# Kernel tuning notes

Measured on AMD Instinct MI355X. Metric: run time of the kernel, lower is better.

Reference implementation:

```python
import jax, jax.numpy as jnp
import numpy as np

V, E, HID, T = 50000, 256, 512, 12   # vocab, embed dim, lstm hidden (bi total), tagset size
START, STOP = 10, 11
L = 2048                              # sentence length
H = HID // 2                          # per-direction hidden
NEG = -10000.0


def setup_inputs():
    key = jax.random.key(0)
    ks = jax.random.split(key, 13)
    s = 0.05
    sentence = jax.random.randint(ks[0], (L,), 0, V)
    embed = jax.random.normal(ks[1], (V, E), jnp.float32) * s
    w_ih_f = jax.random.normal(ks[2], (4 * H, E), jnp.float32) * s
    w_hh_f = jax.random.normal(ks[3], (4 * H, H), jnp.float32) * s
    b_ih_f = jax.random.normal(ks[4], (4 * H,), jnp.float32) * s
    b_hh_f = jax.random.normal(ks[5], (4 * H,), jnp.float32) * s
    w_ih_b = jax.random.normal(ks[6], (4 * H, E), jnp.float32) * s
    w_hh_b = jax.random.normal(ks[7], (4 * H, H), jnp.float32) * s
    b_ih_b = jax.random.normal(ks[8], (4 * H,), jnp.float32) * s
    b_hh_b = jax.random.normal(ks[9], (4 * H,), jnp.float32) * s
    w_out = jax.random.normal(ks[10], (T, HID), jnp.float32) * s
    b_out = jax.random.normal(ks[11], (T,), jnp.float32) * s
    transitions = jax.random.normal(ks[12], (T, T), jnp.float32)
    transitions = transitions.at[START, :].set(NEG).at[:, STOP].set(NEG)
    return dict(sentence=sentence, embed=embed,
                w_ih_f=w_ih_f, w_hh_f=w_hh_f, b_ih_f=b_ih_f, b_hh_f=b_hh_f,
                w_ih_b=w_ih_b, w_hh_b=w_hh_b, b_ih_b=b_ih_b, b_hh_b=b_hh_b,
                w_out=w_out, b_out=b_out, transitions=transitions)


def _lstm_dir(x, w_ih, w_hh, b, reverse):
    # x: [L, E] -> hs: [L, H]; PyTorch gate order i, f, g, o
    xg = x @ w_ih.T + b  # [L, 4H] precomputed input contribution

    def step(carry, xg_t):
        h, c = carry
        g = xg_t + h @ w_hh.T
        i, f, gg, o = jnp.split(g, 4)
        i, f, o = jax.nn.sigmoid(i), jax.nn.sigmoid(f), jax.nn.sigmoid(o)
        c = f * c + i * jnp.tanh(gg)
        h = o * jnp.tanh(c)
        return (h, c), h

    hdim = w_hh.shape[1]
    init = (jnp.zeros((hdim,), x.dtype), jnp.zeros((hdim,), x.dtype))
    _, hs = jax.lax.scan(step, init, xg, reverse=reverse)
    return hs


def _lstm_feats(sentence, embed, w_ih_f, w_hh_f, b_ih_f, b_hh_f,
                w_ih_b, w_hh_b, b_ih_b, b_hh_b, w_out, b_out):
    x = embed[sentence]                                        # [L, E]
    hf = _lstm_dir(x, w_ih_f, w_hh_f, b_ih_f + b_hh_f, False)  # [L, H]
    hb = _lstm_dir(x, w_ih_b, w_hh_b, b_ih_b + b_hh_b, True)   # [L, H]
    h = jnp.concatenate([hf, hb], axis=-1)                     # [L, 2H]
    return h @ w_out.T + b_out                                 # [L, T]


def reference(sentence, embed, w_ih_f, w_hh_f, b_ih_f, b_hh_f,
              w_ih_b, w_hh_b, b_ih_b, b_hh_b, w_out, b_out, transitions):
    feats = _lstm_feats(sentence, embed, w_ih_f, w_hh_f, b_ih_f, b_hh_f,
                        w_ih_b, w_hh_b, b_ih_b, b_hh_b, w_out, b_out)

    # Viterbi DP vectorized over tags, scanned over time
    init_v = jnp.full((T,), NEG, feats.dtype).at[START].set(0.0)

    def vstep(v, feat):
        scores = transitions + v[None, :]        # [next_tag, prev_tag]
        bp = jnp.argmax(scores, axis=1)          # best previous tag per next tag
        v_new = jnp.max(scores, axis=1) + feat
        return v_new, bp

    v, bps = jax.lax.scan(vstep, init_v, feats)  # bps: [L, T]
    terminal = v + transitions[STOP]
    best = jnp.argmax(terminal)
    path_score = terminal[best]

    def btrack(tag, bp):
        return bp[tag], tag

    _, best_path = jax.lax.scan(btrack, best, bps, reverse=True)  # [L] tags
    return path_score, best_path
```

## Files before the change

kernel.cpp:

```cpp
#include <hip/hip_runtime.h>

#define LSEQ 2048
#define TAGS 12

typedef _Float16 half2v __attribute__((ext_vector_type(2)));
typedef unsigned long long u64;

__device__ __forceinline__ float sigm(float x){ return 1.0f/(1.0f+__expf(-x)); }
__device__ __forceinline__ float tanh_fast(float x){ return 1.0f - 2.0f/(1.0f+__expf(2.0f*x)); }
__device__ __forceinline__ half2v pack2(float a, float b){
  half2v r; r.x=(_Float16)a; r.y=(_Float16)b; return r;
}

__device__ __forceinline__ void wg_barrier(){
  asm volatile("s_waitcnt lgkmcnt(0)" ::: "memory");
  __builtin_amdgcn_s_barrier();
  __builtin_amdgcn_sched_barrier(0);
  asm volatile("" ::: "memory");
}

__global__ void init_kernel(u64* ex)
{
  int tid = blockIdx.x*256 + threadIdx.x;
  if (tid < 1024) ex[tid] = 0ull;
}

__global__ void xg_kernel(
    const int* sent, const float* embed,
    const float* w_ih_f, const float* b_ih_f, const float* b_hh_f,
    const float* w_ih_b, const float* b_ih_b, const float* b_hh_b,
    float* xg)
{
  __shared__ float x_sh[8][256];
  int tid = threadIdx.x;
  int t0 = blockIdx.x * 8;
  for (int i=0;i<8;++i){
    int idx = sent[t0+i];
    x_sh[i][tid] = embed[(size_t)idx*256 + tid];
  }
  __syncthreads();
  for (int ri=0; ri<8; ++ri){
    int r = ri*256 + tid;
    int d = r >> 10;
    int row = r & 1023;
    const float* wr = (d ? w_ih_b : w_ih_f) + (size_t)row*256;
    const float* bi = d ? b_ih_b : b_ih_f;
    const float* bh = d ? b_hh_b : b_hh_f;
    float acc[8];
    #pragma unroll
    for (int i=0;i<8;++i) acc[i]=0.f;
    for (int k0=0;k0<256;k0+=4){
      float4 p = *(const float4*)(wr + k0);
      #pragma unroll
      for (int i=0;i<8;++i){
        acc[i] += p.x*x_sh[i][k0] + p.y*x_sh[i][k0+1]
                + p.z*x_sh[i][k0+2] + p.w*x_sh[i][k0+3];
      }
    }
    float bias = bi[row] + bh[row];
    #pragma unroll
    for (int i=0;i<8;++i)
      xg[((size_t)d*LSEQ + (size_t)(t0+i))*1024 + row] = acc[i] + bias;
  }
}

__global__ __launch_bounds__(256,1) void lstm_rec(
    const float* __restrict__ w_hh_f, const float* __restrict__ w_hh_b,
    const float* __restrict__ xg, unsigned short* __restrict__ hstH,
    u64* __restrict__ ex)
{
  int blk = blockIdx.x;
  int d = blk & 7;
  if (d > 1) return;
  int q = blk >> 3;
  int qa = (q+1)&3, qb = (q+2)&3, qc = (q+3)&3;

  int tid = threadIdx.x;
  int g = tid >> 6, l = tid & 63;
  int row = g*256 + 64*q + l;
  const float* W = d ? w_hh_b : w_hh_f;
  const float* xgd = xg + (size_t)d*LSEQ*1024;
  unsigned short* hd = hstH + (size_t)d*LSEQ*256;
  u64* exd = ex + (size_t)d*256;

  __shared__ float gate_sh[2][256];
  __shared__ unsigned h2all[128];

  half2v w[128];
  {
    const float* p0 = W + (size_t)row*256 + 64*q;
    const float* p1 = W + (size_t)row*256 + 64*qa;
    const float* p2 = W + (size_t)row*256 + 64*qb;
    const float* p3 = W + (size_t)row*256 + 64*qc;
    #pragma unroll
    for (int k0=0;k0<16;++k0){
      float4 a = *(const float4*)(p0+4*k0);
      w[2*k0]      = pack2(a.x,a.y);  w[2*k0+1]    = pack2(a.z,a.w);
      float4 b = *(const float4*)(p1+4*k0);
      w[32+2*k0]   = pack2(b.x,b.y);  w[32+2*k0+1] = pack2(b.z,b.w);
      float4 cc= *(const float4*)(p2+4*k0);
      w[64+2*k0]   = pack2(cc.x,cc.y); w[64+2*k0+1] = pack2(cc.z,cc.w);
      float4 e = *(const float4*)(p3+4*k0);
      w[96+2*k0]   = pack2(e.x,e.y);  w[96+2*k0+1] = pack2(e.z,e.w);
    }
  }
  if (tid < 128) h2all[tid] = 0u;
  float c0 = 0.f, c1 = 0.f;
  unsigned hp = 0u;

  int pollj = tid - 64;
  int pollpeer = (q + 1 + (pollj>>5)) & 3;
  int pollslot = 32*pollpeer + (pollj & 31);
  int adrA = (l < 32) ? (32*qa + l) : (32*qb + (l-32));
  int adrB = 32*qc + (l & 31);
  bool is_pub  = (tid < 32);
  bool is_poll = (tid >= 64) && (tid < 160);
  __syncthreads();

  int tf = d ? (LSEQ-1) : 0;
  float xg0 = xgd[(size_t)tf*1024 + row];

  for (int s=0;s<LSEQ;++s){
    u64 v0 = 0ull;
    bool p = is_poll && (s > 0);
    if (p)
      v0 = __hip_atomic_load(&exd[((s&1)<<7) + pollslot],
                             __ATOMIC_RELAXED, __HIP_MEMORY_SCOPE_AGENT);
    float a0=xg0, a1=0.f, a2=0.f, a3=0.f;
    #pragma unroll
    for (int k=0;k<32;k+=4){
      unsigned p0v = __builtin_amdgcn_readlane(hp,k);
      unsigned p1v = __builtin_amdgcn_readlane(hp,k+1);
      unsigned p2v = __builtin_amdgcn_readlane(hp,k+2);
      unsigned p3v = __builtin_amdgcn_readlane(hp,k+3);
      a0 = __builtin_amdgcn_fdot2(__builtin_bit_cast(half2v,p0v), w[k],   a0, false);
      a1 = __builtin_amdgcn_fdot2(__builtin_bit_cast(half2v,p1v), w[k+1], a1, false);
      a2 = __builtin_amdgcn_fdot2(__builtin_bit_cast(half2v,p2v), w[k+2], a2, false);
      a3 = __builtin_amdgcn_fdot2(__builtin_bit_cast(half2v,p3v), w[k+3], a3, false);
    }
    float nxg = 0.f;
    if (s+1 < LSEQ){
      int tn = d ? (LSEQ-2-s) : (s+1);
      nxg = xgd[(size_t)tn*1024 + row];
    }
    if (p){
      u64 v = v0;
      while ((unsigned)(v>>32) != (unsigned)s)
        v = __hip_atomic_load(&exd[((s&1)<<7) + pollslot],
                              __ATOMIC_RELAXED, __HIP_MEMORY_SCOPE_AGENT);
      h2all[pollslot] = (unsigned)v;
    }
    wg_barrier();
    unsigned hrA = h2all[adrA];
    unsigned hrB = h2all[adrB];
    #pragma unroll
    for (int k=0;k<32;k+=2){
      unsigned pA0 = __builtin_amdgcn_readlane(hrA, k);
      unsigned pA1 = __builtin_amdgcn_readlane(hrA, k+1);
      unsigned pB0 = __builtin_amdgcn_readlane(hrA, 32+k);
      unsigned pB1 = __builtin_amdgcn_readlane(hrA, 32+k+1);
      unsigned pC0 = __builtin_amdgcn_readlane(hrB, k);
      unsigned pC1 = __builtin_amdgcn_readlane(hrB, k+1);
      a0 = __builtin_amdgcn_fdot2(__builtin_bit_cast(half2v,pA0), w[32+k],   a0, false);
      a1 = __builtin_amdgcn_fdot2(__builtin_bit_cast(half2v,pA1), w[32+k+1], a1, false);
      a2 = __builtin_amdgcn_fdot2(__builtin_bit_cast(half2v,pB0), w[64+k],   a2, false);
      a3 = __builtin_amdgcn_fdot2(__builtin_bit_cast(half2v,pB1), w[64+k+1], a3, false);
      a0 = __builtin_amdgcn_fdot2(__builtin_bit_cast(half2v,pC0), w[96+k],   a0, false);
      a1 = __builtin_amdgcn_fdot2(__builtin_bit_cast(half2v,pC1), w[96+k+1], a1, false);
    }
    float pre = (a0+a1) + (a2+a3);
    float act = (g==2) ? tanh_fast(pre) : sigm(pre);
    gate_sh[s&1][tid] = act;
    wg_barrier();
    {
      int m = l & 31;
      const float* gp = gate_sh[s&1];
      float2 gi = *(const float2*)&gp[      2*m];
      float2 gf = *(const float2*)&gp[ 64 + 2*m];
      float2 gg = *(const float2*)&gp[128 + 2*m];
      float2 go = *(const float2*)&gp[192 + 2*m];
      c0 = gf.x*c0 + gi.x*gg.x;
      c1 = gf.y*c1 + gi.y*gg.y;
      float h0 = go.x * tanh_fast(c0);
      float h1 = go.y * tanh_fast(c1);
      hp = __builtin_bit_cast(unsigned, pack2(h0,h1));
    }
    if (is_pub){
      if (s+1 < LSEQ)
        atomicExch(&exd[(((s+1)&1)<<7) + 32*q + tid],
                   ((u64)(unsigned)(s+1) << 32) | (u64)hp);
      int tp = d ? (LSEQ-1-s) : s;
      *(unsigned*)&hd[(size_t)tp*256 + 64*q + 2*tid] = hp;
    }
    xg0 = nxg;
  }
}

__global__ void feats_kernel(
    const unsigned short* hstH, const float* w_out, const float* b_out,
    float* feats)
{
  __shared__ float w_sh[12*520];
  __shared__ float h_sh[16*520];
  const _Float16* hf = (const _Float16*)hstH;
  int tid=threadIdx.x;
  int t0=blockIdx.x*16;
  for (int i=tid;i<12*512;i+=256){ int tag=i>>9,k=i&511; w_sh[tag*520+k]=w_out[i]; }
  for (int i=tid;i<16*512;i+=256){
    int tt=i>>9,k=i&511;
    float v = (k<256)? (float)hf[(size_t)(t0+tt)*256+k]
                     : (float)hf[(size_t)(LSEQ+t0+tt)*256 + (k-256)];
    h_sh[tt*520+k]=v;
  }
  __syncthreads();
  if (tid<192){
    int tt=tid/12, tag=tid%12;
    const float* wr=&w_sh[tag*520];
    const float* hr=&h_sh[tt*520];
    float acc=b_out[tag];
    for (int k=0;k<512;k+=4){
      float4 a=*(const float4*)(wr+k);
      float4 b=*(const float4*)(hr+k);
      acc += a.x*b.x+a.y*b.y+a.z*b.z+a.w*b.w;
    }
    feats[(size_t)(t0+tt)*12+tag]=acc;
  }
}

__global__ void BiLSTM_CRF_14405320311361_kernel(
    const float* feats, const float* trans, float* outp)
{
  __shared__ float fsh[LSEQ*12];
  __shared__ unsigned char bps[LSEQ*12];
  __shared__ float term_sh[16];
  __shared__ int ibuf[66];
  __shared__ unsigned char fmap[64*12];
  int tid = threadIdx.x;
  for (int i=tid; i<LSEQ*12/4; i+=256)
    *(float4*)&fsh[4*i] = *(const float4*)&feats[4*i];
  __syncthreads();

  int lane = tid & 63;
  int fl = (lane<12) ? lane : 0;
  float vn = 0.f;
  if (tid < 64){
    float tr[12];
    #pragma unroll
    for (int p=0;p<12;++p) tr[p] = trans[fl*12+p];
    vn = (lane==10) ? 0.f : -10000.f;
    float fa = fsh[fl];
    float fb = fsh[12+fl];
    for (int t=0;t<LSEQ;++t){
      unsigned vu = __float_as_uint(vn);
      float best; int bp; float sc;
      best = tr[0] + __uint_as_float(__builtin_amdgcn_readlane(vu,0)); bp = 0;
      sc = tr[1]  + __uint_as_float(__builtin_amdgcn_readlane(vu,1));  if(sc>best){best=sc;bp=1;}
      sc = tr[2]  + __uint_as_float(__builtin_amdgcn_readlane(vu,2));  if(sc>best){best=sc;bp=2;}
      sc = tr[3]  + __uint_as_float(__builtin_amdgcn_readlane(vu,3));  if(sc>best){best=sc;bp=3;}
      sc = tr[4]  + __uint_as_float(__builtin_amdgcn_readlane(vu,4));  if(sc>best){best=sc;bp=4;}
      sc = tr[5]  + __uint_as_float(__builtin_amdgcn_readlane(vu,5));  if(sc>best){best=sc;bp=5;}
      sc = tr[6]  + __uint_as_float(__builtin_amdgcn_readlane(vu,6));  if(sc>best){best=sc;bp=6;}
      sc = tr[7]  + __uint_as_float(__builtin_amdgcn_readlane(vu,7));  if(sc>best){best=sc;bp=7;}
      sc = tr[8]  + __uint_as_float(__builtin_amdgcn_readlane(vu,8));  if(sc>best){best=sc;bp=8;}
      sc = tr[9]  + __uint_as_float(__builtin_amdgcn_readlane(vu,9));  if(sc>best){best=sc;bp=9;}
      sc = tr[10] + __uint_as_float(__builtin_amdgcn_readlane(vu,10)); if(sc>best){best=sc;bp=10;}
      sc = tr[11] + __uint_as_float(__builtin_amdgcn_readlane(vu,11)); if(sc>best){best=sc;bp=11;}
      vn = best + fa;
      fa = fb;
      if (t+2 < LSEQ) fb = fsh[(t+2)*12+fl];
      if (lane<12) bps[t*12+lane] = (unsigned char)bp;
    }
  }
  if (tid < 12) term_sh[tid] = vn + trans[11*12+tid];
  __syncthreads();
  if (tid == 0){
    float bs=term_sh[0]; int bt=0;
    for (int p=1;p<12;++p){ if (term_sh[p]>bs){bs=term_sh[p];bt=p;} }
    outp[0] = bs;
    ibuf[64] = bt;
  }
  __syncthreads();
  if (tid < 64){
    int b = tid;
    int f[12];
    int thi = b*32+31;
    #pragma unroll
    for (int x=0;x<12;++x) f[x] = bps[thi*12+x];
    for (int t=thi-1; t>=b*32; --t){
      int base = t*12;
      #pragma unroll
      for (int x=0;x<12;++x) f[x] = bps[base + f[x]];
    }
    #pragma unroll
    for (int x=0;x<12;++x) fmap[b*12+x] = (unsigned char)f[x];
  }
  __syncthreads();
  if (tid == 0){
    int tag = ibuf[64];
    for (int b=63;b>=0;--b){ ibuf[b]=tag; tag = fmap[b*12+tag]; }
  }
  __syncthreads();
  if (tid < 64){
    int b = tid;
    int tag = ibuf[b];
    for (int t=b*32+31; t>=b*32; --t){
      outp[1+t] = (float)tag;
      tag = bps[t*12+tag];
    }
  }
}

extern "C" void kernel_launch(void* const* d_in, const int* in_sizes, int n_in,
                              void* d_out, int out_size, void* d_ws, size_t ws_size,
                              hipStream_t stream) {
  const int*   sent   = (const int*)d_in[0];
  const float* embed  = (const float*)d_in[1];
  const float* w_ih_f = (const float*)d_in[2];
  const float* w_hh_f = (const float*)d_in[3];
  const float* b_ih_f = (const float*)d_in[4];
  const float* b_hh_f = (const float*)d_in[5];
  const float* w_ih_b = (const float*)d_in[6];
  const float* w_hh_b = (const float*)d_in[7];
  const float* b_ih_b = (const float*)d_in[8];
  const float* b_hh_b = (const float*)d_in[9];
  const float* w_out  = (const float*)d_in[10];
  const float* b_out  = (const float*)d_in[11];
  const float* trans  = (const float*)d_in[12];

  float* xg = (float*)d_ws;
  unsigned short* hstH = (unsigned short*)(xg + (size_t)2*LSEQ*1024);
  u64* ex = (u64*)(hstH + (size_t)2*LSEQ*256);
  float* feats = (float*)(ex + 1024);
  float* outp  = (float*)d_out;

  init_kernel<<<dim3(4), dim3(256), 0, stream>>>(ex);
  xg_kernel<<<dim3(LSEQ/8), dim3(256), 0, stream>>>(
      sent, embed, w_ih_f, b_ih_f, b_hh_f, w_ih_b, b_ih_b, b_hh_b, xg);
  lstm_rec<<<dim3(32), dim3(256), 0, stream>>>(w_hh_f, w_hh_b, xg, hstH, ex);
  feats_kernel<<<dim3(LSEQ/16), dim3(256), 0, stream>>>(hstH, w_out, b_out, feats);
  BiLSTM_CRF_14405320311361_kernel<<<dim3(1), dim3(256), 0, stream>>>(feats, trans, outp);
}
```

Measured before the change: 3.577 ms.

## Split LSTM recurrence across two workgroups per direction with LDS-resident weight spill

Reduces the recurrent LSTM from four cooperating workgroups per direction to two, each owning 128 hidden units and computing two gate rows per thread. The remote half of the hidden state is exchanged through one global flag/data slot per lane instead of three peers, so cross-workgroup sync traffic and fan-in shrink. Register-held weights only partly fit, so 96 of the remote-half weight columns per row are stored in LDS as packed fp16 and read each step. The cost is more dot-product work per thread and LDS reads on the critical path, traded for fewer inter-block handshakes.

```diff
diff --git a/kernel.cpp b/kernel.cpp
--- a/kernel.cpp
+++ b/kernel.cpp
@@ -4,6 +4,7 @@
 #define TAGS 12
 
 typedef _Float16 half2v __attribute__((ext_vector_type(2)));
+typedef unsigned u32x4 __attribute__((ext_vector_type(4)));
 typedef unsigned long long u64;
 
 __device__ __forceinline__ float sigm(float x){ return 1.0f/(1.0f+__expf(-x)); }
@@ -11,6 +12,7 @@
 __device__ __forceinline__ half2v pack2(float a, float b){
   half2v r; r.x=(_Float16)a; r.y=(_Float16)b; return r;
 }
+__device__ __forceinline__ half2v h2(unsigned u){ return __builtin_bit_cast(half2v, u); }
 
 __device__ __forceinline__ void wg_barrier(){
   asm volatile("s_waitcnt lgkmcnt(0)" ::: "memory");
@@ -72,113 +74,137 @@
   int blk = blockIdx.x;
   int d = blk & 7;
   if (d > 1) return;
-  int q = blk >> 3;
-  int qa = (q+1)&3, qb = (q+2)&3, qc = (q+3)&3;
-
+  int c = blk >> 3;
   int tid = threadIdx.x;
-  int g = tid >> 6, l = tid & 63;
-  int row = g*256 + 64*q + l;
+  int uu = tid & 127;
+  int gp = tid >> 7;
+  int l  = tid & 63;
+  int u  = 128*c + uu;
+  int row0 = gp*256 + u;
+  int row1 = (gp+2)*256 + u;
+  int lr0 = gp*128 + uu;
+  int lr1 = (gp+2)*128 + uu;
   const float* W = d ? w_hh_b : w_hh_f;
   const float* xgd = xg + (size_t)d*LSEQ*1024;
   unsigned short* hd = hstH + (size_t)d*LSEQ*256;
   u64* exd = ex + (size_t)d*256;
 
-  __shared__ float gate_sh[2][256];
-  __shared__ unsigned h2all[128];
-
-  half2v w[128];
+  __shared__ unsigned wlds[12][512][4];
+  __shared__ float gate_sh[2][512];
+  __shared__ unsigned h2rem[2][64];
+
+  half2v wA[80], wB[80];
   {
-    const float* p0 = W + (size_t)row*256 + 64*q;
-    const float* p1 = W + (size_t)row*256 + 64*qa;
-    const float* p2 = W + (size_t)row*256 + 64*qb;
-    const float* p3 = W + (size_t)row*256 + 64*qc;
-    #pragma unroll
-    for (int k0=0;k0<16;++k0){
-      float4 a = *(const float4*)(p0+4*k0);
-      w[2*k0]      = pack2(a.x,a.y);  w[2*k0+1]    = pack2(a.z,a.w);
-      float4 b = *(const float4*)(p1+4*k0);
-      w[32+2*k0]   = pack2(b.x,b.y);  w[32+2*k0+1] = pack2(b.z,b.w);
-      float4 cc= *(const float4*)(p2+4*k0);
-      w[64+2*k0]   = pack2(cc.x,cc.y); w[64+2*k0+1] = pack2(cc.z,cc.w);
-      float4 e = *(const float4*)(p3+4*k0);
-      w[96+2*k0]   = pack2(e.x,e.y);  w[96+2*k0+1] = pack2(e.z,e.w);
-    }
-  }
-  if (tid < 128) h2all[tid] = 0u;
+    const float* pr0 = W + (size_t)row0*256;
+    const float* pr1 = W + (size_t)row1*256;
+    int ob = 128*c, pb = 128*(1-c);
+    #pragma unroll
+    for (int k2=0;k2<32;++k2){
+      float4 a = *(const float4*)(pr0 + ob + 4*k2);
+      wA[2*k2] = pack2(a.x,a.y); wA[2*k2+1] = pack2(a.z,a.w);
+      float4 b = *(const float4*)(pr1 + ob + 4*k2);
+      wB[2*k2] = pack2(b.x,b.y); wB[2*k2+1] = pack2(b.z,b.w);
+    }
+    #pragma unroll
+    for (int k2=0;k2<8;++k2){
+      float4 a = *(const float4*)(pr0 + pb + 4*k2);
+      wA[64+2*k2] = pack2(a.x,a.y); wA[64+2*k2+1] = pack2(a.z,a.w);
+      float4 b = *(const float4*)(pr1 + pb + 4*k2);
+      wB[64+2*k2] = pack2(b.x,b.y); wB[64+2*k2+1] = pack2(b.z,b.w);
+    }
+    for (int jg=0;jg<12;++jg){
+      float4 a0 = *(const float4*)(pr0 + pb + 32 + 8*jg);
+      float4 a1 = *(const float4*)(pr0 + pb + 32 + 8*jg + 4);
+      wlds[jg][lr0][0] = __builtin_bit_cast(unsigned, pack2(a0.x,a0.y));
+      wlds[jg][lr0][1] = __builtin_bit_cast(unsigned, pack2(a0.z,a0.w));
+      wlds[jg][lr0][2] = __builtin_bit_cast(unsigned, pack2(a1.x,a1.y));
+      wlds[jg][lr0][3] = __builtin_bit_cast(unsigned, pack2(a1.z,a1.w));
+      float4 b0 = *(const float4*)(pr1 + pb + 32 + 8*jg);
+      float4 b1 = *(const float4*)(pr1 + pb + 32 + 8*jg + 4);
+      wlds[jg][lr1][0] = __builtin_bit_cast(unsigned, pack2(b0.x,b0.y));
+      wlds[jg][lr1][1] = __builtin_bit_cast(unsigned, pack2(b0.z,b0.w));
+      wlds[jg][lr1][2] = __builtin_bit_cast(unsigned, pack2(b1.x,b1.y));
+      wlds[jg][lr1][3] = __builtin_bit_cast(unsigned, pack2(b1.z,b1.w));
+    }
+  }
+  if (tid < 128) h2rem[tid>>6][tid&63] = 0u;
   float c0 = 0.f, c1 = 0.f;
   unsigned hp = 0u;
-
-  int pollj = tid - 64;
-  int pollpeer = (q + 1 + (pollj>>5)) & 3;
-  int pollslot = 32*pollpeer + (pollj & 31);
-  int adrA = (l < 32) ? (32*qa + l) : (32*qb + (l-32));
-  int adrB = 32*qc + (l & 31);
-  bool is_pub  = (tid < 32);
-  bool is_poll = (tid >= 64) && (tid < 160);
+  bool is_pub  = (tid < 64);
+  bool is_poll = (tid >= 64) && (tid < 128);
   __syncthreads();
 
   int tf = d ? (LSEQ-1) : 0;
-  float xg0 = xgd[(size_t)tf*1024 + row];
+  float xga = xgd[(size_t)tf*1024 + row0];
+  float xgb = xgd[(size_t)tf*1024 + row1];
 
   for (int s=0;s<LSEQ;++s){
+    int par = s & 1;
+    bool p = is_poll && (s > 0);
     u64 v0 = 0ull;
-    bool p = is_poll && (s > 0);
     if (p)
-      v0 = __hip_atomic_load(&exd[((s&1)<<7) + pollslot],
+      v0 = __hip_atomic_load(&exd[par*128 + (1-c)*64 + l],
                              __ATOMIC_RELAXED, __HIP_MEMORY_SCOPE_AGENT);
-    float a0=xg0, a1=0.f, a2=0.f, a3=0.f;
-    #pragma unroll
-    for (int k=0;k<32;k+=4){
-      unsigned p0v = __builtin_amdgcn_readlane(hp,k);
-      unsigned p1v = __builtin_amdgcn_readlane(hp,k+1);
-      unsigned p2v = __builtin_amdgcn_readlane(hp,k+2);
-      unsigned p3v = __builtin_amdgcn_readlane(hp,k+3);
-      a0 = __builtin_amdgcn_fdot2(__builtin_bit_cast(half2v,p0v), w[k],   a0, false);
-      a1 = __builtin_amdgcn_fdot2(__builtin_bit_cast(half2v,p1v), w[k+1], a1, false);
-      a2 = __builtin_amdgcn_fdot2(__builtin_bit_cast(half2v,p2v), w[k+2], a2, false);
-      a3 = __builtin_amdgcn_fdot2(__builtin_bit_cast(half2v,p3v), w[k+3], a3, false);
-    }
-    float nxg = 0.f;
-    if (s+1 < LSEQ){
-      int tn = d ? (LSEQ-2-s) : (s+1);
-      nxg = xgd[(size_t)tn*1024 + row];
-    }
+    float a0 = xga, a1 = xgb, b0 = 0.f, b1 = 0.f;
+    #pragma unroll
+    for (int k=0;k<64;k+=2){
+      unsigned h0v = __builtin_amdgcn_readlane(hp, k);
+      unsigned h1v = __builtin_amdgcn_readlane(hp, k+1);
+      a0 = __builtin_amdgcn_fdot2(h2(h0v), wA[k],   a0, false);
+      a1 = __builtin_amdgcn_fdot2(h2(h0v), wB[k],   a1, false);
+      b0 = __builtin_amdgcn_fdot2(h2(h1v), wA[k+1], b0, false);
+      b1 = __builtin_amdgcn_fdot2(h2(h1v), wB[k+1], b1, false);
+    }
+    int tn = (s+1 < LSEQ) ? (d ? (LSEQ-2-s) : (s+1)) : tf;
+    float nxa = xgd[(size_t)tn*1024 + row0];
+    float nxb = xgd[(size_t)tn*1024 + row1];
     if (p){
       u64 v = v0;
       while ((unsigned)(v>>32) != (unsigned)s)
-        v = __hip_atomic_load(&exd[((s&1)<<7) + pollslot],
+        v = __hip_atomic_load(&exd[par*128 + (1-c)*64 + l],
                               __ATOMIC_RELAXED, __HIP_MEMORY_SCOPE_AGENT);
-      h2all[pollslot] = (unsigned)v;
+      h2rem[par][l] = (unsigned)v;
     }
     wg_barrier();
-    unsigned hrA = h2all[adrA];
-    unsigned hrB = h2all[adrB];
-    #pragma unroll
-    for (int k=0;k<32;k+=2){
-      unsigned pA0 = __builtin_amdgcn_readlane(hrA, k);
-      unsigned pA1 = __builtin_amdgcn_readlane(hrA, k+1);
-      unsigned pB0 = __builtin_amdgcn_readlane(hrA, 32+k);
-      unsigned pB1 = __builtin_amdgcn_readlane(hrA, 32+k+1);
-      unsigned pC0 = __builtin_amdgcn_readlane(hrB, k);
-      unsigned pC1 = __builtin_amdgcn_readlane(hrB, k+1);
-      a0 = __builtin_amdgcn_fdot2(__builtin_bit_cast(half2v,pA0), w[32+k],   a0, false);
-      a1 = __builtin_amdgcn_fdot2(__builtin_bit_cast(half2v,pA1), w[32+k+1], a1, false);
-      a2 = __builtin_amdgcn_fdot2(__builtin_bit_cast(half2v,pB0), w[64+k],   a2, false);
-      a3 = __builtin_amdgcn_fdot2(__builtin_bit_cast(half2v,pB1), w[64+k+1], a3, false);
-      a0 = __builtin_amdgcn_fdot2(__builtin_bit_cast(half2v,pC0), w[96+k],   a0, false);
-      a1 = __builtin_amdgcn_fdot2(__builtin_bit_cast(half2v,pC1), w[96+k+1], a1, false);
-    }
-    float pre = (a0+a1) + (a2+a3);
-    float act = (g==2) ? tanh_fast(pre) : sigm(pre);
-    gate_sh[s&1][tid] = act;
+    unsigned hr = h2rem[par][l];
+    #pragma unroll
+    for (int k=0;k<16;k+=2){
+      unsigned h0v = __builtin_amdgcn_readlane(hr, k);
+      unsigned h1v = __builtin_amdgcn_readlane(hr, k+1);
+      a0 = __builtin_amdgcn_fdot2(h2(h0v), wA[64+k],   a0, false);
+      a1 = __builtin_amdgcn_fdot2(h2(h0v), wB[64+k],   a1, false);
+      b0 = __builtin_amdgcn_fdot2(h2(h1v), wA[64+k+1], b0, false);
+      b1 = __builtin_amdgcn_fdot2(h2(h1v), wB[64+k+1], b1, false);
+    }
+    #pragma unroll
+    for (int jg=0;jg<12;++jg){
+      u32x4 ga = *(const u32x4*)&wlds[jg][lr0][0];
+      u32x4 gb = *(const u32x4*)&wlds[jg][lr1][0];
+      unsigned h0v = __builtin_amdgcn_readlane(hr, 16+4*jg);
+      unsigned h1v = __builtin_amdgcn_readlane(hr, 17+4*jg);
+      unsigned h2v = __builtin_amdgcn_readlane(hr, 18+4*jg);
+      unsigned h3v = __builtin_amdgcn_readlane(hr, 19+4*jg);
+      a0 = __builtin_amdgcn_fdot2(h2(h0v), h2(ga[0]), a0, false);
+      a1 = __builtin_amdgcn_fdot2(h2(h0v), h2(gb[0]), a1, false);
+      b0 = __builtin_amdgcn_fdot2(h2(h1v), h2(ga[1]), b0, false);
+      b1 = __builtin_amdgcn_fdot2(h2(h1v), h2(gb[1]), b1, false);
+      a0 = __builtin_amdgcn_fdot2(h2(h2v), h2(ga[2]), a0, false);
+      a1 = __builtin_amdgcn_fdot2(h2(h2v), h2(gb[2]), a1, false);
+      b0 = __builtin_amdgcn_fdot2(h2(h3v), h2(ga[3]), b0, false);
+      b1 = __builtin_amdgcn_fdot2(h2(h3v), h2(gb[3]), b1, false);
+    }
+    float pre0 = a0 + b0, pre1 = a1 + b1;
+    float act0 = sigm(pre0);
+    float act1 = (gp==0) ? tanh_fast(pre1) : sigm(pre1);
+    gate_sh[par][gp*128 + uu]     = act0;
+    gate_sh[par][(gp+2)*128 + uu] = act1;
     wg_barrier();
     {
-      int m = l & 31;
-      const float* gp = gate_sh[s&1];
-      float2 gi = *(const float2*)&gp[      2*m];
-      float2 gf = *(const float2*)&gp[ 64 + 2*m];
-      float2 gg = *(const float2*)&gp[128 + 2*m];
-      float2 go = *(const float2*)&gp[192 + 2*m];
+      const float* gpt = gate_sh[par];
+      float2 gi = *(const float2*)&gpt[      2*l];
+      float2 gf = *(const float2*)&gpt[128 + 2*l];
+      float2 gg = *(const float2*)&gpt[256 + 2*l];
+      float2 go = *(const float2*)&gpt[384 + 2*l];
       c0 = gf.x*c0 + gi.x*gg.x;
       c1 = gf.y*c1 + gi.y*gg.y;
       float h0 = go.x * tanh_fast(c0);
@@ -187,12 +213,12 @@
     }
     if (is_pub){
       if (s+1 < LSEQ)
-        atomicExch(&exd[(((s+1)&1)<<7) + 32*q + tid],
+        atomicExch(&exd[(((s+1)&1))*128 + c*64 + l],
                    ((u64)(unsigned)(s+1) << 32) | (u64)hp);
       int tp = d ? (LSEQ-1-s) : s;
-      *(unsigned*)&hd[(size_t)tp*256 + 64*q + 2*tid] = hp;
-    }
-    xg0 = nxg;
+      *(unsigned*)&hd[(size_t)tp*256 + 128*c + 2*l] = hp;
+    }
+    xga = nxa; xgb = nxb;
   }
 }
 
@@ -336,7 +362,7 @@
   init_kernel<<<dim3(4), dim3(256), 0, stream>>>(ex);
   xg_kernel<<<dim3(LSEQ/8), dim3(256), 0, stream>>>(
       sent, embed, w_ih_f, b_ih_f, b_hh_f, w_ih_b, b_ih_b, b_hh_b, xg);
-  lstm_rec<<<dim3(32), dim3(256), 0, stream>>>(w_hh_f, w_hh_b, xg, hstH, ex);
+  lstm_rec<<<dim3(16), dim3(256), 0, stream>>>(w_hh_f, w_hh_b, xg, hstH, ex);
   feats_kernel<<<dim3(LSEQ/16), dim3(256), 0, stream>>>(hstH, w_out, b_out, feats);
   BiLSTM_CRF_14405320311361_kernel<<<dim3(1), dim3(256), 0, stream>>>(feats, trans, outp);
 }
```

Result: slower. 4.769 ms (+33.3%).
